# Optimization experiments

Hardware: AMD Instinct MI355X
Metric: run time of the kernel (lower is better)

Reference implementation:

```python
import jax, jax.numpy as jnp
import numpy as np

T, B, C, H, W = 4, 16, 256, 32, 32
NH = 8  # num_heads
CH = C // NH
N = H * W
EPS = 1e-5

# Heaviside spike with ATan surrogate gradient (spikingjelly default, alpha=2.0)
@jax.custom_vjp
def spike(x):
    return (x >= 0.0).astype(x.dtype)

def _spike_fwd(x):
    return spike(x), x

def _spike_bwd(x, g):
    alpha = 2.0
    return (g * (alpha / 2.0) / (1.0 + (jnp.pi / 2.0 * alpha * x) ** 2),)

spike.defvjp(_spike_fwd, _spike_bwd)

def lif(x_seq, tau, v_th):
    """Multi-step LIF over leading time axis. v_reset=0 hard reset, detach_reset."""
    def step(v, xt):
        h = v + (xt - v) / tau            # charge
        s = spike(h - v_th)               # fire
        v_next = h * (1.0 - jax.lax.stop_gradient(s))  # hard reset to 0, detached
        return v_next, s
    v0 = jnp.zeros_like(x_seq[0])
    _, spikes = jax.lax.scan(step, v0, x_seq)
    return spikes

def bn1d(x, gamma, beta, mean, var):
    # x: [T,B,C,N]; per-channel affine norm (eval-mode BatchNorm1d)
    inv = gamma / jnp.sqrt(var + EPS)
    return (x - mean[None, None, :, None]) * inv[None, None, :, None] + beta[None, None, :, None]

def setup_inputs() -> dict:
    key = jax.random.key(0)
    ks = jax.random.split(key, 16)
    d = {
        'x': jax.random.normal(ks[0], (T, B, C, H, W), jnp.float32),
        'q_w': jax.random.normal(ks[1], (C, C), jnp.float32) * 0.05,
        'q_gamma': jax.random.uniform(ks[2], (C,), jnp.float32),
        'q_beta': jax.random.normal(ks[3], (C,), jnp.float32) * 0.1,
        'q_mean': jax.random.normal(ks[4], (C,), jnp.float32) * 0.1,
        'q_var': jax.random.uniform(ks[5], (C,), jnp.float32) + 0.5,
        'k_w': jax.random.normal(ks[6], (C, C), jnp.float32) * 0.05,
        'k_gamma': jax.random.uniform(ks[7], (C,), jnp.float32),
        'k_beta': jax.random.normal(ks[8], (C,), jnp.float32) * 0.1,
        'k_mean': jax.random.normal(ks[9], (C,), jnp.float32) * 0.1,
        'k_var': jax.random.uniform(ks[10], (C,), jnp.float32) + 0.5,
        'proj_w': jax.random.normal(ks[11], (C, C), jnp.float32) * 0.05,
        'proj_b': jax.random.normal(ks[12], (C,), jnp.float32) * 0.1,
        'p_gamma': jax.random.uniform(ks[13], (C,), jnp.float32),
        'p_beta': jax.random.normal(ks[14], (C,), jnp.float32) * 0.1,
        'p_mean': jax.random.normal(ks[15], (C,), jnp.float32) * 0.1,
        'p_var': jax.random.uniform(jax.random.fold_in(key, 99), (C,), jnp.float32) + 0.5,
    }
    return d

def reference(x, q_w, q_gamma, q_beta, q_mean, q_var,
              k_w, k_gamma, k_beta, k_mean, k_var,
              proj_w, proj_b, p_gamma, p_beta, p_mean, p_var):
    xn = x.reshape(T, B, C, N)  # flatten spatial
    # q branch: 1x1 conv == channel matmul, then BN, then push/pull LIF
    q = bn1d(jnp.einsum('oc,tbcn->tbon', q_w, xn), q_gamma, q_beta, q_mean, q_var)
    qe_s = lif(q, 2.0, 1.0)   # excitatory spikes
    qi_s = lif(-q, 2.0, 1.0)  # inhibitory spikes
    qe = qe_s.reshape(T, B, NH, CH, N)
    qi = qi_s.reshape(T, B, NH, CH, N)
    # k branch
    k = bn1d(jnp.einsum('oc,tbcn->tbon', k_w, xn), k_gamma, k_beta, k_mean, k_var)
    k_s = lif(k, 2.0, 1.0).reshape(T, B, NH, CH, N)
    # push-pull linear attention: sum over head-channel dim, then LIF gate
    qe_sum = jnp.sum(qe, axis=3, keepdims=True)  # [T,B,NH,1,N]
    qi_sum = jnp.sum(qi, axis=3, keepdims=True)
    attn = lif(qe_sum - qi_sum, 2.0, 0.5)        # v_threshold=0.5
    x_one = attn * k_s                            # [T,B,NH,CH,N]
    xo = x_one.reshape(T, B, C, N)
    # projection: 1x1 conv with bias + BN
    p = jnp.einsum('oc,tbcn->tbon', proj_w, xo) + proj_b[None, None, :, None]
    p = bn1d(p, p_gamma, p_beta, p_mean, p_var).reshape(T, B, C, H, W)
    x_final = lif(p, 2.0, 1.0)
    return x_final
```

## Files before the change

### kernel.cpp

```cpp
#include <hip/hip_runtime.h>
#include <math.h>
#include <stdint.h>

#define TT 4
#define BB 16
#define CC 256
#define NN 1024
#define NT 16
#define EPSF 1e-5f
#define EPS_R 1e-5f

typedef __attribute__((ext_vector_type(8))) short short8;
typedef __attribute__((ext_vector_type(4))) float f32x4;
#define MFMA __builtin_amdgcn_mfma_f32_16x16x32_bf16

#define XCH 1040
#define XPL 33280
#define LDS_X 0
#define LDS_XF 99840
#define LDS_TOT 134656

__device__ __forceinline__ uint32_t f2bf(float x) {
  const uint32_t u = __float_as_uint(x);
  return (u + 0x7FFFu + ((u >> 16) & 1u)) >> 16;
}
__device__ __forceinline__ float bf2f(uint32_t b) { return __uint_as_float(b << 16); }

__global__ __launch_bounds__(256)
void wsplit2(const float* __restrict__ qw, const float* __restrict__ kw,
             const float* __restrict__ pw, uint16_t* __restrict__ ws) {
  const int gid = blockIdx.x * 256 + threadIdx.x;
  const int mat = gid >> 13;
  const int ot  = (gid >> 9) & 15;
  const int kk  = (gid >> 6) & 7;
  const int l   = gid & 63;
  const float* w = (mat == 0 ? qw : (mat == 1 ? kw : pw));
  const int o  = ot * 16 + (l & 15);
  const int k0 = kk * 32 + (l >> 4) * 8;
  uint16_t ph[8], pm[8], pl[8];
  #pragma unroll
  for (int j = 0; j < 8; ++j) {
    const float v = w[(size_t)o * CC + k0 + j];
    const uint32_t bh = f2bf(v);
    const float r1 = v - bf2f(bh);
    const uint32_t bm = f2bf(r1);
    const float r2 = r1 - bf2f(bm);
    ph[j] = (uint16_t)bh; pm[j] = (uint16_t)bm; pl[j] = (uint16_t)f2bf(r2);
  }
  const size_t base = ((size_t)mat * 3 * 65536) + ((size_t)ot * 4096) +
                      kk * 512 + l * 8;
  *(uint4*)(ws + base)          = *(const uint4*)ph;
  *(uint4*)(ws + base + 65536)  = *(const uint4*)pm;
  *(uint4*)(ws + base + 131072) = *(const uint4*)pl;
}

__device__ __forceinline__ void lif4m(float q0, float q1, float q2, float q3,
                                      float th, float s[4], float& mg) {
  const float qq[4] = {q0, q1, q2, q3};
  float v = 0.f;
  #pragma unroll
  for (int t = 0; t < 4; ++t) {
    const float h = v + (qq[t] - v) * 0.5f;
    const float d = h - th;
    mg = fminf(mg, fabsf(d));
    const bool f = d >= 0.f;
    s[t] = f ? 1.f : 0.f;
    v = f ? 0.f : h;
  }
}

__device__ __forceinline__ void rescue3(const float* __restrict__ wrow,
                                        const char* lds, int ln, float sv[4]) {
  #pragma unroll
  for (int t = 0; t < 4; ++t) sv[t] = 0.f;
  #pragma unroll 1
  for (int c8 = 0; c8 < 32; ++c8) {
    const float4 wa = *(const float4*)(wrow + c8 * 8);
    const float4 wb = *(const float4*)(wrow + c8 * 8 + 4);
    const float wl_[8] = {wa.x, wa.y, wa.z, wa.w, wb.x, wb.y, wb.z, wb.w};
    #pragma unroll
    for (int t = 0; t < 4; ++t) {
      const int off = c8 * XCH + (t * 16 + ln) * 16;
      const short8 h = *(const short8*)(lds + LDS_X + 0 * XPL + off);
      const short8 m = *(const short8*)(lds + LDS_X + 1 * XPL + off);
      const short8 l = *(const short8*)(lds + LDS_X + 2 * XPL + off);
      float s = sv[t];
      #pragma unroll
      for (int j = 0; j < 8; ++j) {
        const float xv = (bf2f((uint16_t)h[j]) + bf2f((uint16_t)m[j])) +
                         bf2f((uint16_t)l[j]);
        s = fmaf(wl_[j], xv, s);
      }
      sv[t] = s;
    }
  }
}

__device__ __forceinline__ void rescue1(const float* __restrict__ wrow,
                                        const char* lds, int ln, float sv[4]) {
  #pragma unroll
  for (int t = 0; t < 4; ++t) sv[t] = 0.f;
  #pragma unroll 1
  for (int c8 = 0; c8 < 32; ++c8) {
    const float4 wa = *(const float4*)(wrow + c8 * 8);
    const float4 wb = *(const float4*)(wrow + c8 * 8 + 4);
    const float wl_[8] = {wa.x, wa.y, wa.z, wa.w, wb.x, wb.y, wb.z, wb.w};
    #pragma unroll
    for (int t = 0; t < 4; ++t) {
      const int off = c8 * XCH + (t * 16 + ln) * 16;
      const short8 h = *(const short8*)(lds + LDS_X + off);
      float s = sv[t];
      #pragma unroll
      for (int j = 0; j < 8; ++j)
        s = fmaf(wl_[j], bf2f((uint16_t)h[j]), s);
      sv[t] = s;
    }
  }
}

__global__ __launch_bounds__(1024, 4)
void pushpull_mfma4(const float* __restrict__ x,
                    const float* __restrict__ q_w, const float* __restrict__ q_gamma,
                    const float* __restrict__ q_beta, const float* __restrict__ q_mean,
                    const float* __restrict__ q_var,
                    const float* __restrict__ k_w, const float* __restrict__ k_gamma,
                    const float* __restrict__ k_beta, const float* __restrict__ k_mean,
                    const float* __restrict__ k_var,
                    const float* __restrict__ proj_w, const float* __restrict__ proj_b,
                    const float* __restrict__ p_gamma, const float* __restrict__ p_beta,
                    const float* __restrict__ p_mean, const float* __restrict__ p_var,
                    const uint16_t* __restrict__ ws, float* __restrict__ out) {
  __shared__ __align__(16) char lds[LDS_TOT];

  const int tid  = threadIdx.x;
  const int bid  = (int)blockIdx.x;
  const int lid  = ((bid & 7) << 7) | (bid >> 3);
  const int b    = lid >> 6;
  const int n0   = (lid & 63) * NT;
  const int lane = tid & 63;
  const int ln   = tid & 15;
  const int g    = (tid >> 4) & 3;
  const int ot   = tid >> 6;

  float* xf = (float*)(lds + LDS_XF);
  #pragma unroll 1
  for (int hb = 0; hb < 2; ++hb) {
    #pragma unroll
    for (int it = 0; it < 2; ++it) {
      const int idx = it * 1024 + tid;
      const int n4 = (idx & 3) * 4, t = (idx >> 2) & 3, cl = idx >> 4;
      const float4 v = *(const float4*)(
          x + ((size_t)(t * BB + b) * CC + hb * 128 + cl) * NN + n0 + n4);
      *(float4*)(xf + cl * 68 + t * 16 + n4) = v;
    }
    __syncthreads();
    {
      const int chL = tid >> 6, col = tid & 63;
      uint16_t ph[8], pm[8], pl[8];
      #pragma unroll
      for (int j = 0; j < 8; ++j) {
        const float v = xf[(chL * 8 + j) * 68 + col];
        const uint32_t bh = f2bf(v);
        const float r1 = v - bf2f(bh);
        const uint32_t bm = f2bf(r1);
        const float r2 = r1 - bf2f(bm);
        ph[j] = (uint16_t)bh; pm[j] = (uint16_t)bm; pl[j] = (uint16_t)f2bf(r2);
      }
      const int ca = (hb * 16 + chL) * XCH + col * 16;
      *(uint4*)(lds + LDS_X + 0 * XPL + ca) = *(const uint4*)ph;
      *(uint4*)(lds + LDS_X + 1 * XPL + ca) = *(const uint4*)pm;
      *(uint4*)(lds + LDS_X + 2 * XPL + ca) = *(const uint4*)pl;
    }
    __syncthreads();
  }

  const char* wq = (const char*)ws;
  const char* wk = (const char*)ws + 393216;
  const char* wp = (const char*)ws + 786432;

  f32x4 aq[4], ak[4];
  #pragma unroll
  for (int nt = 0; nt < 4; ++nt) { aq[nt] = (f32x4)0.f; ak[nt] = (f32x4)0.f; }
  #pragma unroll 1
  for (int kk = 0; kk < 8; ++kk) {
    short8 fq[3], fk[3];
    #pragma unroll
    for (int p = 0; p < 3; ++p) {
      const size_t foff = (size_t)p * 131072 + (size_t)ot * 8192 + kk * 1024 + lane * 16;
      fq[p] = *(const short8*)(wq + foff);
      fk[p] = *(const short8*)(wk + foff);
    }
    #pragma unroll
    for (int nt = 0; nt < 4; ++nt) {
      const int boff = (kk * 4 + g) * XCH + (nt * 16 + ln) * 16;
      const short8 b0 = *(const short8*)(lds + LDS_X + 0 * XPL + boff);
      const short8 b1 = *(const short8*)(lds + LDS_X + 1 * XPL + boff);
      const short8 b2 = *(const short8*)(lds + LDS_X + 2 * XPL + boff);
      aq[nt] = MFMA(fq[2], b0, aq[nt], 0, 0, 0);
      aq[nt] = MFMA(fq[1], b1, aq[nt], 0, 0, 0);
      aq[nt] = MFMA(fq[0], b2, aq[nt], 0, 0, 0);
      aq[nt] = MFMA(fq[1], b0, aq[nt], 0, 0, 0);
      aq[nt] = MFMA(fq[0], b1, aq[nt], 0, 0, 0);
      aq[nt] = MFMA(fq[0], b0, aq[nt], 0, 0, 0);
      ak[nt] = MFMA(fk[2], b0, ak[nt], 0, 0, 0);
      ak[nt] = MFMA(fk[1], b1, ak[nt], 0, 0, 0);
      ak[nt] = MFMA(fk[0], b2, ak[nt], 0, 0, 0);
      ak[nt] = MFMA(fk[1], b0, ak[nt], 0, 0, 0);
      ak[nt] = MFMA(fk[0], b1, ak[nt], 0, 0, 0);
      ak[nt] = MFMA(fk[0], b0, ak[nt], 0, 0, 0);
    }
  }

  float dsum[4] = {0.f, 0.f, 0.f, 0.f};
  #pragma unroll
  for (int r = 0; r < 4; ++r) {
    const int o = ot * 16 + g * 4 + r;
    const float inv = q_gamma[o] / sqrtf(q_var[o] + EPSF);
    const float mn = q_mean[o], bt = q_beta[o];
    float qv[4];
    #pragma unroll
    for (int t = 0; t < 4; ++t) qv[t] = (aq[t][r] - mn) * inv + bt;
    float se[4], si[4], mg = 1e30f;
    lif4m(qv[0], qv[1], qv[2], qv[3], 1.0f, se, mg);
    lif4m(-qv[0], -qv[1], -qv[2], -qv[3], 1.0f, si, mg);
    if (__builtin_expect(mg < EPS_R, 0)) {
      float qx[4];
      rescue3(q_w + (size_t)o * CC, lds, ln, qx);
      #pragma unroll
      for (int t = 0; t < 4; ++t) qx[t] = (qx[t] - mn) * inv + bt;
      float m2 = 1e30f;
      lif4m(qx[0], qx[1], qx[2], qx[3], 1.0f, se, m2);
      lif4m(-qx[0], -qx[1], -qx[2], -qx[3], 1.0f, si, m2);
    }
    #pragma unroll
    for (int t = 0; t < 4; ++t) dsum[t] += se[t] - si[t];
  }
  #pragma unroll
  for (int t = 0; t < 4; ++t) {
    float v = dsum[t];
    v += __shfl_xor(v, 16);
    v += __shfl_xor(v, 32);
    dsum[t] = v;
  }

  unsigned kb = 0u;
  #pragma unroll
  for (int r = 0; r < 4; ++r) {
    const int o = ot * 16 + g * 4 + r;
    const float inv = k_gamma[o] / sqrtf(k_var[o] + EPSF);
    const float mn = k_mean[o], bt = k_beta[o];
    float kv[4];
    #pragma unroll
    for (int t = 0; t < 4; ++t) kv[t] = (ak[t][r] - mn) * inv + bt;
    float sk[4], mg = 1e30f;
    lif4m(kv[0], kv[1], kv[2], kv[3], 1.0f, sk, mg);
    if (__builtin_expect(mg < EPS_R, 0)) {
      float kx[4];
      rescue3(k_w + (size_t)o * CC, lds, ln, kx);
      #pragma unroll
      for (int t = 0; t < 4; ++t) kx[t] = (kx[t] - mn) * inv + bt;
      float m2 = 1e30f;
      lif4m(kx[0], kx[1], kx[2], kx[3], 1.0f, sk, m2);
    }
    #pragma unroll
    for (int t = 0; t < 4; ++t) kb |= (sk[t] != 0.f) ? (1u << (r * 4 + t)) : 0u;
  }

  float* db = (float*)(lds + LDS_XF);
  __syncthreads();
  if (g == 0) {
    #pragma unroll
    for (int t = 0; t < 4; ++t) db[(ot * 16 + ln) * 4 + t] = dsum[t];
  }
  __syncthreads();
  float at[4];
  {
    float tot[4];
    #pragma unroll
    for (int t = 0; t < 4; ++t)
      tot[t] = dsum[t] + db[((ot ^ 1) * 16 + ln) * 4 + t];
    float mgd = 1e30f;
    lif4m(tot[0], tot[1], tot[2], tot[3], 0.5f, at, mgd);
  }

  {
    const int chunk = ot * 2 + (g >> 1);
    const int j0 = (g & 1) * 4;
    #pragma unroll
    for (int t = 0; t < 4; ++t) {
      unsigned long long wbits = 0ull;
      #pragma unroll
      for (int r = 0; r < 4; ++r)
        if (((kb >> (r * 4 + t)) & 1u) && at[t] != 0.f)
          wbits |= 0x3F80ull << (r * 16);
      *(unsigned long long*)(lds + LDS_X + chunk * XCH +
                             (t * 16 + ln) * 16 + j0 * 2) = wbits;
    }
  }
  __syncthreads();

  f32x4 ap[4];
  #pragma unroll
  for (int nt = 0; nt < 4; ++nt) ap[nt] = (f32x4)0.f;
  #pragma unroll 1
  for (int kk = 0; kk < 8; ++kk) {
    short8 fp_[3];
    #pragma unroll
    for (int p = 0; p < 3; ++p)
      fp_[p] = *(const short8*)(wp + (size_t)p * 131072 + (size_t)ot * 8192 +
                                kk * 1024 + lane * 16);
    #pragma unroll
    for (int nt = 0; nt < 4; ++nt) {
      const short8 b0 = *(const short8*)(lds + LDS_X +
                                         (kk * 4 + g) * XCH + (nt * 16 + ln) * 16);
      ap[nt] = MFMA(fp_[2], b0, ap[nt], 0, 0, 0);
      ap[nt] = MFMA(fp_[1], b0, ap[nt], 0, 0, 0);
      ap[nt] = MFMA(fp_[0], b0, ap[nt], 0, 0, 0);
    }
  }

  #pragma unroll
  for (int r = 0; r < 4; ++r) {
    const int o = ot * 16 + g * 4 + r;
    const float inv = p_gamma[o] / sqrtf(p_var[o] + EPSF);
    const float mn = p_mean[o], bt = p_beta[o], pb = proj_b[o];
    float pv[4];
    #pragma unroll
    for (int t = 0; t < 4; ++t) pv[t] = ((ap[t][r] + pb) - mn) * inv + bt;
    float sp[4], mg = 1e30f;
    lif4m(pv[0], pv[1], pv[2], pv[3], 1.0f, sp, mg);
    if (__builtin_expect(mg < EPS_R, 0)) {
      float px[4];
      rescue1(proj_w + (size_t)o * CC, lds, ln, px);
      #pragma unroll
      for (int t = 0; t < 4; ++t) px[t] = ((px[t] + pb) - mn) * inv + bt;
      float m2 = 1e30f;
      lif4m(px[0], px[1], px[2], px[3], 1.0f, sp, m2);
    }
    #pragma unroll
    for (int t = 0; t < 4; ++t)
      out[((size_t)(t * BB + b) * CC + o) * NN + n0 + ln] = sp[t];
  }
}

extern "C" void kernel_launch(void* const* d_in, const int* in_sizes, int n_in,
                              void* d_out, int out_size, void* d_ws, size_t ws_size,
                              hipStream_t stream) {
  const float* x       = (const float*)d_in[0];
  const float* q_w     = (const float*)d_in[1];
  const float* q_gamma = (const float*)d_in[2];
  const float* q_beta  = (const float*)d_in[3];
  const float* q_mean  = (const float*)d_in[4];
  const float* q_var   = (const float*)d_in[5];
  const float* k_w     = (const float*)d_in[6];
  const float* k_gamma = (const float*)d_in[7];
  const float* k_beta  = (const float*)d_in[8];
  const float* k_mean  = (const float*)d_in[9];
  const float* k_var   = (const float*)d_in[10];
  const float* proj_w  = (const float*)d_in[11];
  const float* proj_b  = (const float*)d_in[12];
  const float* p_gamma = (const float*)d_in[13];
  const float* p_beta  = (const float*)d_in[14];
  const float* p_mean  = (const float*)d_in[15];
  const float* p_var   = (const float*)d_in[16];
  float* out = (float*)d_out;
  uint16_t* wsp = (uint16_t*)d_ws;

  wsplit2<<<96, 256, 0, stream>>>(q_w, k_w, proj_w, wsp);
  pushpull_mfma4<<<BB * (NN / NT), 1024, 0, stream>>>(
      x, q_w, q_gamma, q_beta, q_mean, q_var,
      k_w, k_gamma, k_beta, k_mean, k_var,
      proj_w, proj_b, p_gamma, p_beta, p_mean, p_var, wsp, out);
}
```

Measured before the change: 155.4 us.

## Drop to two-term bf16 split, shrink LDS, rescue near-threshold from global fp32

Switches the activation and weight bf16 splitting from three terms to two, cutting the MFMA count per tile from 6 to 3 for q/k and from 3 to 2 for proj. The smaller split shrinks LDS enough to raise the occupancy hint to 8 waves per EU, and x staging now runs in 8 smaller chunks. The near-threshold rescue path reads fp32 x from global memory, and its margin is widened to make up for the lower precision. The wider margin means the slow rescue path fires more often, and s_setprio calls are added around the MFMA loops.

Result: slower. 447.5 us (+187.9%).

```diff
diff --git a/kernel.cpp b/kernel.cpp
--- a/kernel.cpp
+++ b/kernel.cpp
@@ -8,7 +8,7 @@
 #define NN 1024
 #define NT 16
 #define EPSF 1e-5f
-#define EPS_R 1e-5f
+#define EPS_R 6e-5f
 
 typedef __attribute__((ext_vector_type(8))) short short8;
 typedef __attribute__((ext_vector_type(4))) float f32x4;
@@ -17,8 +17,8 @@
 #define XCH 1040
 #define XPL 33280
 #define LDS_X 0
-#define LDS_XF 99840
-#define LDS_TOT 134656
+#define LDS_XF 66560
+#define LDS_TOT 75008
 
 __device__ __forceinline__ uint32_t f2bf(float x) {
   const uint32_t u = __float_as_uint(x);
@@ -69,7 +69,20 @@
   }
 }
 
-__device__ __forceinline__ void rescue3(const float* __restrict__ wrow,
+__device__ __forceinline__ void rescue3g(const float* __restrict__ wrow,
+                                         const float* __restrict__ x,
+                                         int b, int n0, int ln, float sv[4]) {
+  #pragma unroll
+  for (int t = 0; t < 4; ++t) {
+    const float* xg = x + (size_t)(t * BB + b) * CC * NN + n0 + ln;
+    float s = 0.f;
+    #pragma unroll 1
+    for (int c = 0; c < CC; ++c) s = fmaf(wrow[c], xg[(size_t)c * NN], s);
+    sv[t] = s;
+  }
+}
+
+__device__ __forceinline__ void rescue1(const float* __restrict__ wrow,
                                         const char* lds, int ln, float sv[4]) {
   #pragma unroll
   for (int t = 0; t < 4; ++t) sv[t] = 0.f;
@@ -81,33 +94,6 @@
     #pragma unroll
     for (int t = 0; t < 4; ++t) {
       const int off = c8 * XCH + (t * 16 + ln) * 16;
-      const short8 h = *(const short8*)(lds + LDS_X + 0 * XPL + off);
-      const short8 m = *(const short8*)(lds + LDS_X + 1 * XPL + off);
-      const short8 l = *(const short8*)(lds + LDS_X + 2 * XPL + off);
-      float s = sv[t];
-      #pragma unroll
-      for (int j = 0; j < 8; ++j) {
-        const float xv = (bf2f((uint16_t)h[j]) + bf2f((uint16_t)m[j])) +
-                         bf2f((uint16_t)l[j]);
-        s = fmaf(wl_[j], xv, s);
-      }
-      sv[t] = s;
-    }
-  }
-}
-
-__device__ __forceinline__ void rescue1(const float* __restrict__ wrow,
-                                        const char* lds, int ln, float sv[4]) {
-  #pragma unroll
-  for (int t = 0; t < 4; ++t) sv[t] = 0.f;
-  #pragma unroll 1
-  for (int c8 = 0; c8 < 32; ++c8) {
-    const float4 wa = *(const float4*)(wrow + c8 * 8);
-    const float4 wb = *(const float4*)(wrow + c8 * 8 + 4);
-    const float wl_[8] = {wa.x, wa.y, wa.z, wa.w, wb.x, wb.y, wb.z, wb.w};
-    #pragma unroll
-    for (int t = 0; t < 4; ++t) {
-      const int off = c8 * XCH + (t * 16 + ln) * 16;
       const short8 h = *(const short8*)(lds + LDS_X + off);
       float s = sv[t];
       #pragma unroll
@@ -118,8 +104,8 @@
   }
 }
 
-__global__ __launch_bounds__(1024, 4)
-void pushpull_mfma4(const float* __restrict__ x,
+__global__ __launch_bounds__(1024, 8)
+void pushpull_mfma7(const float* __restrict__ x,
                     const float* __restrict__ q_w, const float* __restrict__ q_gamma,
                     const float* __restrict__ q_beta, const float* __restrict__ q_mean,
                     const float* __restrict__ q_var,
@@ -144,32 +130,27 @@
 
   float* xf = (float*)(lds + LDS_XF);
   #pragma unroll 1
-  for (int hb = 0; hb < 2; ++hb) {
-    #pragma unroll
-    for (int it = 0; it < 2; ++it) {
-      const int idx = it * 1024 + tid;
-      const int n4 = (idx & 3) * 4, t = (idx >> 2) & 3, cl = idx >> 4;
+  for (int ps = 0; ps < 8; ++ps) {
+    if (tid < 512) {
+      const int cl = tid >> 4, t = (tid >> 2) & 3, n4 = (tid & 3) * 4;
       const float4 v = *(const float4*)(
-          x + ((size_t)(t * BB + b) * CC + hb * 128 + cl) * NN + n0 + n4);
-      *(float4*)(xf + cl * 68 + t * 16 + n4) = v;
+          x + ((size_t)(t * BB + b) * CC + ps * 32 + cl) * NN + n0 + n4);
+      *(float4*)(xf + cl * 66 + t * 16 + n4) = v;
     }
     __syncthreads();
-    {
+    if (tid < 256) {
       const int chL = tid >> 6, col = tid & 63;
-      uint16_t ph[8], pm[8], pl[8];
+      uint16_t ph[8], pm[8];
       #pragma unroll
       for (int j = 0; j < 8; ++j) {
-        const float v = xf[(chL * 8 + j) * 68 + col];
+        const float v = xf[(chL * 8 + j) * 66 + col];
         const uint32_t bh = f2bf(v);
-        const float r1 = v - bf2f(bh);
-        const uint32_t bm = f2bf(r1);
-        const float r2 = r1 - bf2f(bm);
-        ph[j] = (uint16_t)bh; pm[j] = (uint16_t)bm; pl[j] = (uint16_t)f2bf(r2);
+        pm[j] = (uint16_t)f2bf(v - bf2f(bh));
+        ph[j] = (uint16_t)bh;
       }
-      const int ca = (hb * 16 + chL) * XCH + col * 16;
-      *(uint4*)(lds + LDS_X + 0 * XPL + ca) = *(const uint4*)ph;
-      *(uint4*)(lds + LDS_X + 1 * XPL + ca) = *(const uint4*)pm;
-      *(uint4*)(lds + LDS_X + 2 * XPL + ca) = *(const uint4*)pl;
+      const int ca = (ps * 4 + chL) * XCH + col * 16;
+      *(uint4*)(lds + LDS_X + ca) = *(const uint4*)ph;
+      *(uint4*)(lds + LDS_X + XPL + ca) = *(const uint4*)pm;
     }
     __syncthreads();
   }
@@ -183,32 +164,28 @@
   for (int nt = 0; nt < 4; ++nt) { aq[nt] = (f32x4)0.f; ak[nt] = (f32x4)0.f; }
   #pragma unroll 1
   for (int kk = 0; kk < 8; ++kk) {
-    short8 fq[3], fk[3];
-    #pragma unroll
-    for (int p = 0; p < 3; ++p) {
-      const size_t foff = (size_t)p * 131072 + (size_t)ot * 8192 + kk * 1024 + lane * 16;
+    short8 fq[2], fk[2];
+    #pragma unroll
+    for (int p = 0; p < 2; ++p) {
+      const size_t foff = (size_t)p * 131072 + (size_t)ot * 8192 +
+                          (size_t)kk * 1024 + (size_t)lane * 16;
       fq[p] = *(const short8*)(wq + foff);
       fk[p] = *(const short8*)(wk + foff);
     }
+    __builtin_amdgcn_s_setprio(1);
     #pragma unroll
     for (int nt = 0; nt < 4; ++nt) {
       const int boff = (kk * 4 + g) * XCH + (nt * 16 + ln) * 16;
-      const short8 b0 = *(const short8*)(lds + LDS_X + 0 * XPL + boff);
-      const short8 b1 = *(const short8*)(lds + LDS_X + 1 * XPL + boff);
-      const short8 b2 = *(const short8*)(lds + LDS_X + 2 * XPL + boff);
-      aq[nt] = MFMA(fq[2], b0, aq[nt], 0, 0, 0);
-      aq[nt] = MFMA(fq[1], b1, aq[nt], 0, 0, 0);
-      aq[nt] = MFMA(fq[0], b2, aq[nt], 0, 0, 0);
+      const short8 b0 = *(const short8*)(lds + LDS_X + boff);
+      const short8 b1 = *(const short8*)(lds + LDS_X + XPL + boff);
       aq[nt] = MFMA(fq[1], b0, aq[nt], 0, 0, 0);
       aq[nt] = MFMA(fq[0], b1, aq[nt], 0, 0, 0);
       aq[nt] = MFMA(fq[0], b0, aq[nt], 0, 0, 0);
-      ak[nt] = MFMA(fk[2], b0, ak[nt], 0, 0, 0);
-      ak[nt] = MFMA(fk[1], b1, ak[nt], 0, 0, 0);
-      ak[nt] = MFMA(fk[0], b2, ak[nt], 0, 0, 0);
       ak[nt] = MFMA(fk[1], b0, ak[nt], 0, 0, 0);
       ak[nt] = MFMA(fk[0], b1, ak[nt], 0, 0, 0);
       ak[nt] = MFMA(fk[0], b0, ak[nt], 0, 0, 0);
     }
+    __builtin_amdgcn_s_setprio(0);
   }
 
   float dsum[4] = {0.f, 0.f, 0.f, 0.f};
@@ -225,7 +202,7 @@
     lif4m(-qv[0], -qv[1], -qv[2], -qv[3], 1.0f, si, mg);
     if (__builtin_expect(mg < EPS_R, 0)) {
       float qx[4];
-      rescue3(q_w + (size_t)o * CC, lds, ln, qx);
+      rescue3g(q_w + (size_t)o * CC, x, b, n0, ln, qx);
       #pragma unroll
       for (int t = 0; t < 4; ++t) qx[t] = (qx[t] - mn) * inv + bt;
       float m2 = 1e30f;
@@ -256,7 +233,7 @@
     lif4m(kv[0], kv[1], kv[2], kv[3], 1.0f, sk, mg);
     if (__builtin_expect(mg < EPS_R, 0)) {
       float kx[4];
-      rescue3(k_w + (size_t)o * CC, lds, ln, kx);
+      rescue3g(k_w + (size_t)o * CC, x, b, n0, ln, kx);
       #pragma unroll
       for (int t = 0; t < 4; ++t) kx[t] = (kx[t] - mn) * inv + bt;
       float m2 = 1e30f;
@@ -304,19 +281,20 @@
   for (int nt = 0; nt < 4; ++nt) ap[nt] = (f32x4)0.f;
   #pragma unroll 1
   for (int kk = 0; kk < 8; ++kk) {
-    short8 fp_[3];
-    #pragma unroll
-    for (int p = 0; p < 3; ++p)
+    short8 fp_[2];
+    #pragma unroll
+    for (int p = 0; p < 2; ++p)
       fp_[p] = *(const short8*)(wp + (size_t)p * 131072 + (size_t)ot * 8192 +
-                                kk * 1024 + lane * 16);
+                                (size_t)kk * 1024 + (size_t)lane * 16);
+    __builtin_amdgcn_s_setprio(1);
     #pragma unroll
     for (int nt = 0; nt < 4; ++nt) {
       const short8 b0 = *(const short8*)(lds + LDS_X +
-                                         (kk * 4 + g) * XCH + (nt * 16 + ln) * 16);
-      ap[nt] = MFMA(fp_[2], b0, ap[nt], 0, 0, 0);
+                        (kk * 4 + g) * XCH + (nt * 16 + ln) * 16);
       ap[nt] = MFMA(fp_[1], b0, ap[nt], 0, 0, 0);
       ap[nt] = MFMA(fp_[0], b0, ap[nt], 0, 0, 0);
     }
+    __builtin_amdgcn_s_setprio(0);
   }
 
   #pragma unroll
@@ -367,7 +345,7 @@
   uint16_t* wsp = (uint16_t*)d_ws;
 
   wsplit2<<<96, 256, 0, stream>>>(q_w, k_w, proj_w, wsp);
-  pushpull_mfma4<<<BB * (NN / NT), 1024, 0, stream>>>(
+  pushpull_mfma7<<<BB * (NN / NT), 1024, 0, stream>>>(
       x, q_w, q_gamma, q_beta, q_mean, q_var,
       k_w, k_gamma, k_beta, k_mean, k_var,
       proj_w, proj_b, p_gamma, p_beta, p_mean, p_var, wsp, out);
```
